# Kernel optimization log

Hardware: AMD Instinct MI355X
Metric: run time of the kernel (lower is better)

Reference implementation:

```python
import jax, jax.numpy as jnp
import numpy as np

BIT = 128
Y_P = 0.5
RIGHT = BIT / 8.0
LEFT = RIGHT / 2.0
UB = BIT / 2.0
ALPHA = 0.1
PCT_NUM, PCT_DEN = 9, 10  # percent = 9/10
C_COEF = (1.0 / RIGHT) * np.log(Y_P / (99.0 * (1.0 - Y_P)))  # slope c (constant since y_p fixed)
A_COEF = -1.0 / (LEFT * C_COEF) * np.log(99.0 * Y_P / (1.0 - Y_P))  # hard-branch factor a
# with y_p=0.5: d = -c*BP, g = -a*c*BP, so f_easy = c*(x-BP), f_hard = a*c*(x-BP)


def setup_inputs() -> dict:
    key = jax.random.key(0)
    k1, k2 = jax.random.split(key)
    N, C = 6144, 200
    u = jax.random.normal(k1, (N, BIT), dtype=jnp.float32)
    labels = jax.random.randint(k2, (N,), 0, C)
    y = jax.nn.one_hot(labels, C, dtype=jnp.int32)
    ind = jnp.arange(N, dtype=jnp.int32)  # unused dataset indices
    return {"u": u, "y": y, "ind": ind}


def reference(u, y, ind):
    sg = jax.lax.stop_gradient
    N = u.shape[0]
    uh = jnp.tanh(u)
    s = (y @ y.T) > 0                      # [N,N] bool similarity (diagonal is True)
    inner = uh @ uh.T                      # [N,N]
    n_sim = s.sum(axis=1)                  # int per-row similar count
    n_dis = N - n_sim
    fn_sim = n_sim.astype(jnp.float32)
    fn_dis = n_dis.astype(jnp.float32)
    idx = jnp.arange(N)[None, :]

    meanS = jnp.clip(jnp.where(s, inner, 0.0).sum(1) / jnp.maximum(fn_sim, 1.0), 0.0, UB)
    meanDS = jnp.clip(jnp.where(s, 0.0, inner).sum(1) / jnp.maximum(fn_dis, 1.0), 0.0, UB)

    dis_sorted = jnp.sort(jnp.where(s, -jnp.inf, inner), axis=1)
    start_dis = (n_dis * PCT_NUM) // PCT_DEN          # int(len*0.9)
    tail_mask = idx >= (N - n_dis + start_dis)[:, None]
    tail_cnt = jnp.maximum((n_dis - start_dis).astype(jnp.float32), 1.0)
    dMax = jnp.clip(jnp.where(tail_mask, dis_sorted, 0.0).sum(1) / tail_cnt, 0.0, UB)

    sim_sorted = jnp.sort(jnp.where(s, inner, jnp.inf), axis=1)
    start_sim = (n_sim * PCT_NUM) // PCT_DEN
    head_mask = idx < (n_sim - start_sim)[:, None]
    head_cnt = jnp.maximum((n_sim - start_sim).astype(jnp.float32), 1.0)
    sMin = jnp.clip(jnp.where(head_mask, sim_sorted, 0.0).sum(1) / head_cnt, 0.0, UB)

    # .item() in the original detaches these -> stop_gradient
    meanS, meanDS, dMax, sMin = map(sg, (meanS, meanDS, dMax, sMin))
    BP = meanS - (UB - meanS) / UB * jnp.abs(meanS - dMax)      # [N]
    BPd = meanDS + meanDS / UB * jnp.abs(meanDS - sMin)         # [N]

    # similar-pair loss: f + log(1+exp(-f)) == softplus(f)
    dc = inner - BP[:, None]
    f_sim = jnp.where(inner > BP[:, None], C_COEF * dc, A_COEF * C_COEF * dc)
    mask_sim = s & (inner != BP[:, None])             # == BP excluded in torch indexing
    cnt_sim = jnp.maximum(mask_sim.sum(1).astype(jnp.float32), 1.0)
    row_pos = jnp.where(mask_sim, jax.nn.softplus(f_sim), 0.0).sum(1) / cnt_sim

    # dissimilar-pair loss: log(1+exp(-f)) == softplus(-f)
    dcd = inner - BPd[:, None]
    f_dis = jnp.where(inner < BPd[:, None], C_COEF * dcd, A_COEF * C_COEF * dcd)
    mask_dis = (~s) & (inner != BPd[:, None])
    cnt_dis = jnp.maximum(mask_dis.sum(1).astype(jnp.float32), 1.0)
    row_neg = jnp.where(mask_dis, jax.nn.softplus(-f_dis), 0.0).sum(1) / cnt_dis

    valid = (n_sim > 0) & (n_dis > 0)
    count = valid.sum().astype(jnp.float32)
    posL = jnp.where(count > 0, jnp.where(valid, row_pos, 0.0).sum() / jnp.maximum(count, 1.0), 0.0)
    navL = jnp.where(count > 0, jnp.where(valid, row_neg, 0.0).sum() / jnp.maximum(count, 1.0), 0.0)

    q_loss = ALPHA * jnp.mean((uh - jnp.sign(uh)) ** 2)
    return posL + navL + q_loss
```

## Files before the change

kernel.cpp:

```cpp
#include <hip/hip_runtime.h>
#include <cstdint>

#define NROW 6144
#define KDIM 128
#define NLAB 200
#define C_COEF (-0.28719499063341177f)
#define UBV 64.0f

typedef _Float16 f16x8 __attribute__((ext_vector_type(8)));
typedef float f32x4 __attribute__((ext_vector_type(4)));
typedef __attribute__((address_space(1))) const void as1c_void;
typedef __attribute__((address_space(3))) void as3_void;

union U8 { f16x8 h; unsigned u[4]; };
union CV16 { _Float16 h; unsigned short us; };

__device__ __forceinline__ float softplus_f(float x){
  return fmaxf(x, 0.f) + __logf(1.f + __expf(-fabsf(x)));
}
__device__ __forceinline__ float waveRedF(float v){
#pragma unroll
  for (int o = 32; o; o >>= 1) v += __shfl_down(v, o, 64);
  return v;
}
__device__ __forceinline__ float bfRedF(float v){
#pragma unroll
  for (int o = 32; o; o >>= 1) v += __shfl_xor(v, o, 64);
  return v;
}
__device__ __forceinline__ int bfMaxI(int v){
#pragma unroll
  for (int o = 32; o; o >>= 1){ int x = __shfl_xor(v, o, 64); v = v > x ? v : x; }
  return v;
}
__device__ __forceinline__ float bfMaxF(float v){
#pragma unroll
  for (int o = 32; o; o >>= 1) v = fmaxf(v, __shfl_xor(v, o, 64));
  return v;
}
__device__ __forceinline__ float val_of_key(unsigned key){
  unsigned bits = (key & 0x8000u) ? (key ^ 0x8000u) : (key ^ 0xFFFFu);
  CV16 cv; cv.us = (unsigned short)bits;
  return (float)cv.h;
}

__global__ void k_label(const int* __restrict__ y, unsigned char* __restrict__ lab,
                        int* __restrict__ cnt, int* __restrict__ simIdx){
  const int row = blockIdx.x;
  const int t = threadIdx.x;
  if (t < NLAB){
    if (y[(size_t)row * NLAB + t] != 0){
      lab[row] = (unsigned char)t;
      int p = atomicAdd(&cnt[t], 1);
      if (p < 512) simIdx[t * 512 + p] = row;
    }
  }
}

__global__ __launch_bounds__(192) void k_clsmask(const unsigned char* __restrict__ lab,
                                                 unsigned* __restrict__ cm){
  const int c = blockIdx.x;
  const int w = threadIdx.x;
  const uint4* p = (const uint4*)(lab + w * 32);
  uint4 a = p[0], b = p[1];
  unsigned words[8] = {a.x, a.y, a.z, a.w, b.x, b.y, b.z, b.w};
  unsigned bits = 0;
#pragma unroll
  for (int j = 0; j < 8; j++)
#pragma unroll
    for (int i = 0; i < 4; i++)
      if (((words[j] >> (8 * i)) & 255u) == (unsigned)c) bits |= 1u << (4 * j + i);
  cm[c * 192 + w] = bits;
}

__global__ __launch_bounds__(256) void k_tanh(const float* __restrict__ u,
    _Float16* __restrict__ uhswz, float* __restrict__ accf){
  const int tid = threadIdx.x;
  const int gid = blockIdx.x * 256 + tid;
  const int row = gid >> 4;
  const int h = gid & 15;
  const int g = h ^ (row & 7);
  const float* sp = u + (size_t)row * KDIM + g * 8;
  float q = 0.f;
  f16x8 o;
#pragma unroll
  for (int t = 0; t < 8; t++){
    float x = sp[t];
    float e2 = __expf(2.f * x);
    float th = 1.f - 2.f * __builtin_amdgcn_rcpf(e2 + 1.f);
    float sg = (th > 0.f) ? 1.f : ((th < 0.f) ? -1.f : 0.f);
    float d = th - sg;
    q += d * d;
    o[t] = (_Float16)th;
  }
  *(f16x8*)(uhswz + (size_t)row * KDIM + h * 8) = o;
  q = waveRedF(q);
  __shared__ float qb[4];
  if ((tid & 63) == 0) qb[tid >> 6] = q;
  __syncthreads();
  if (tid == 0) atomicAdd(&accf[0], qb[0] + qb[1] + qb[2] + qb[3]);
}

__global__ __launch_bounds__(256) void k_mm(const _Float16* __restrict__ A,
    _Float16* __restrict__ out, int row0){
  __shared__ __align__(16) _Float16 SH[2 * 128 * KDIM];
  _Float16* As = SH;
  _Float16* Bs = SH + 128 * KDIM;
  const int tid = threadIdx.x;
  const int wav = tid >> 6, lane = tid & 63;
  const int bj = blockIdx.x, bi = blockIdx.y;

  const char* Ag = (const char*)(A + (size_t)(row0 + bi * 128) * KDIM);
  const char* Bg = (const char*)(A + (size_t)(bj * 128) * KDIM);
  char* Asb = (char*)As;
  char* Bsb = (char*)Bs;
#pragma unroll
  for (int t = 0; t < 8; t++){
    const int ub = wav * 8192 + t * 1024;
    __builtin_amdgcn_global_load_lds((as1c_void*)(Ag + ub + lane * 16),
                                     (as3_void*)(Asb + ub), 16, 0, 0);
    __builtin_amdgcn_global_load_lds((as1c_void*)(Bg + ub + lane * 16),
                                     (as3_void*)(Bsb + ub), 16, 0, 0);
  }
  __syncthreads();

  const int quad = lane >> 4, l16 = lane & 15;
  const int wm = (wav >> 1) * 64, wn = (wav & 1) * 64;
  f32x4 acc[4][4];
#pragma unroll
  for (int im = 0; im < 4; im++)
#pragma unroll
    for (int in = 0; in < 4; in++)
      acc[im][in] = (f32x4){0.f, 0.f, 0.f, 0.f};

#pragma unroll
  for (int kb = 0; kb < 4; kb++){
    f16x8 af[4], bf[4];
#pragma unroll
    for (int i = 0; i < 4; i++){
      const int m = wm + i * 16 + l16;
      const int gidx = kb * 4 + quad;
      af[i] = *(const f16x8*)(Asb + m * 256 + ((gidx ^ (m & 7)) << 4));
      const int n = wn + i * 16 + l16;
      bf[i] = *(const f16x8*)(Bsb + n * 256 + ((gidx ^ (n & 7)) << 4));
    }
#pragma unroll
    for (int im = 0; im < 4; im++)
#pragma unroll
      for (int in = 0; in < 4; in++)
        acc[im][in] = __builtin_amdgcn_mfma_f32_16x16x32_f16(af[im], bf[in], acc[im][in], 0, 0, 0);
  }
  __syncthreads();

  _Float16* Cs = SH;
#pragma unroll
  for (int im = 0; im < 4; im++)
#pragma unroll
    for (int in = 0; in < 4; in++)
#pragma unroll
      for (int r = 0; r < 4; r++){
        const int rl = wm + im * 16 + quad * 4 + r;
        const int cl = wn + in * 16 + l16;
        Cs[rl * 132 + cl] = (_Float16)acc[im][in][r];
      }
  __syncthreads();

  _Float16* obase = out + (size_t)(bi * 128) * NROW + (size_t)bj * 128;
  const int s = tid & 15;
#pragma unroll
  for (int i = 0; i < 8; i++){
    const int r = (tid >> 4) + i * 16;
    f16x8 vv = *(const f16x8*)(Cs + r * 132 + s * 8);
    *(f16x8*)(obase + (size_t)r * NROW + s * 8) = vv;
  }
}

__global__ __launch_bounds__(256) void k_stats(const _Float16* __restrict__ buf,
    const unsigned char* __restrict__ lab, const int* __restrict__ cnt,
    const int* __restrict__ simIdx, const unsigned* __restrict__ cm,
    float* __restrict__ rowRes, int row0){
  __shared__ int   histS[4][256];
  __shared__ float simvS[4][512];
  const int tid = threadIdx.x;
  const int lane = tid & 63;
  const int wav = tid >> 6;
  const int lrow = blockIdx.x * 4 + wav;
  const int row = row0 + lrow;
  const int myl = lab[row];
  const int n_sim = cnt[myl];
  const int n_dis = NROW - n_sim;
  if (n_dis == 0 || n_sim == 0) return;
  const int k1 = n_dis - (n_dis * 9) / 10;
  const int k2 = n_sim - (n_sim * 9) / 10;
  const int ns = (n_sim < 512) ? n_sim : 512;

  int*   hist = histS[wav];
  float* simv = simvS[wav];
  *(int4*)&hist[lane * 4] = make_int4(0, 0, 0, 0);

  const f16x8* src = (const f16x8*)(buf + (size_t)lrow * NROW);
  const _Float16* srcs = buf + (size_t)lrow * NROW;
  const unsigned char* mrow = (const unsigned char*)(cm + (size_t)myl * 192);

  float sumAll = 0.f;
#pragma unroll 1
  for (int it = 0; it < 12; ++it){
    U8 x; x.h = src[it * 64 + lane];
#pragma unroll
    for (int k = 0; k < 4; k++){
      unsigned wv = x.u[k];
      unsigned m = (wv >> 15) & 0x00010001u;
      unsigned key2 = wv ^ 0x80008000u ^ (m * 0x7FFFu);
      atomicAdd(&hist[(key2 >> 8) & 0xFFu], 1);
      atomicAdd(&hist[key2 >> 24], 1);
      sumAll += (float)x.h[2 * k] + (float)x.h[2 * k + 1];
    }
  }

  float sumS = 0.f;
  unsigned skey[8]; float sval[8];
#pragma unroll
  for (int j = 0; j < 8; j++){
    const int t = lane + 64 * j;
    skey[j] = 0xFFFFFFFFu; sval[j] = 0.f;
    if (t < ns){
      int idx = simIdx[myl * 512 + t];
      CV16 cv; cv.h = srcs[idx];
      unsigned bits = cv.us;
      unsigned key = bits ^ 0x8000u ^ ((bits >> 15) * 0x7FFFu);
      float v = (float)cv.h;
      simv[t] = v; sumS += v;
      atomicAdd(&hist[key >> 8], -1);
      skey[j] = key; sval[j] = v;
    }
  }
  sumAll = bfRedF(sumAll);
  sumS = bfRedF(sumS);
  const float sumD = sumAll - sumS;

  int cArr[4];
  { int4 c4 = *(const int4*)&hist[lane * 4];
    cArr[0] = c4.x; cArr[1] = c4.y; cArr[2] = c4.z; cArr[3] = c4.w; }
  int part = cArr[0] + cArr[1] + cArr[2] + cArr[3];
  int suf = part;
#pragma unroll
  for (int o = 1; o < 64; o <<= 1){
    int x = __shfl_down(suf, o, 64);
    if (lane + o < 64) suf += x;
  }
  int cum = suf - part;
  int encB = -1, krF = 0;
#pragma unroll
  for (int d = 3; d >= 0; --d){
    int cd = cArr[d];
    if (k1 > cum && k1 <= cum + cd){ encB = 4 * lane + d; krF = k1 - cum; }
    cum += cd;
  }
  const int hbStar = bfMaxI(encB);
  const int kr1 = bfMaxI(krF);

  *(int4*)&hist[lane * 4] = make_int4(0, 0, 0, 0);

  float sAb = 0.f;
#pragma unroll 1
  for (int it = 0; it < 12; ++it){
    U8 x; x.h = src[it * 64 + lane];
#pragma unroll
    for (int k = 0; k < 4; k++){
      unsigned wv = x.u[k];
      unsigned m = (wv >> 15) & 0x00010001u;
      unsigned key2 = wv ^ 0x80008000u ^ (m * 0x7FFFu);
      int hbLo = (key2 >> 8) & 0xFF;
      int hbHi = key2 >> 24;
      if (hbLo > hbStar) sAb += (float)x.h[2 * k];
      else if (hbLo == hbStar) atomicAdd(&hist[key2 & 0xFFu], 1);
      if (hbHi > hbStar) sAb += (float)x.h[2 * k + 1];
      else if (hbHi == hbStar) atomicAdd(&hist[(key2 >> 16) & 0xFFu], 1);
    }
  }
#pragma unroll
  for (int j = 0; j < 8; j++){
    if (skey[j] != 0xFFFFFFFFu){
      int hb = (int)(skey[j] >> 8);
      if (hb > hbStar) sAb -= sval[j];
      else if (hb == hbStar) atomicAdd(&hist[skey[j] & 0xFFu], -1);
    }
  }
  sAb = bfRedF(sAb);

  int c2[4];
  { int4 c4 = *(const int4*)&hist[lane * 4];
    c2[0] = c4.x; c2[1] = c4.y; c2[2] = c4.z; c2[3] = c4.w; }
  part = c2[0] + c2[1] + c2[2] + c2[3];
  suf = part;
#pragma unroll
  for (int o = 1; o < 64; o <<= 1){
    int x = __shfl_down(suf, o, 64);
    if (lane + o < 64) suf += x;
  }
  cum = suf - part;
  int encL = -1, g2F = 0;
#pragma unroll
  for (int d = 3; d >= 0; --d){
    int cd = c2[d];
    if (kr1 > cum && kr1 <= cum + cd){ encL = 4 * lane + d; g2F = cum; }
    cum += cd;
  }
  const int lbStar = bfMaxI(encL);
  const int gt2 = bfMaxI(g2F);
  float sumIn = 0.f;
#pragma unroll
  for (int d = 0; d < 4; d++){
    int lb = 4 * lane + d;
    if (lb > lbStar) sumIn += (float)c2[d] * val_of_key((unsigned)((hbStar << 8) | lb));
  }
  sumIn = bfRedF(sumIn);
  const float piv = val_of_key((unsigned)((hbStar << 8) | lbStar));
  const float dSum = sAb + sumIn + (float)(kr1 - gt2) * piv;

  float fpiv2 = -3e38f; int flt = 0;
  for (int t = lane; t < ns; t += 64){
    float vt = simv[t];
    int lt = 0, eq = 0;
    for (int j = 0; j < ns; j++){
      float vj = simv[j];
      lt += (vj < vt); eq += (vj == vt);
    }
    if (lt < k2 && k2 <= lt + eq){ fpiv2 = vt; flt = lt; }
  }
  const float piv2 = bfMaxF(fpiv2);
  const int ltS = bfMaxI(flt);
  float slt = 0.f;
  for (int t = lane; t < ns; t += 64){
    float v = simv[t];
    if (v < piv2) slt += v;
  }
  slt = bfRedF(slt);
  const float sSum = slt + (float)(k2 - ltS) * piv2;

  const float meanS  = fminf(fmaxf(sumS / fmaxf((float)n_sim, 1.f), 0.f), UBV);
  const float meanDS = fminf(fmaxf(sumD / fmaxf((float)n_dis, 1.f), 0.f), UBV);
  const float dMax   = fminf(fmaxf(dSum / fmaxf((float)k1, 1.f), 0.f), UBV);
  const float sMin   = fminf(fmaxf(sSum / fmaxf((float)k2, 1.f), 0.f), UBV);
  const float BP  = meanS - (UBV - meanS) / UBV * fabsf(meanS - dMax);
  const float BPd = meanDS + meanDS / UBV * fabsf(meanDS - sMin);

  float an = 0.f, cn = 0.f;
#pragma unroll 1
  for (int it = 0; it < 12; ++it){
    f16x8 h8 = src[it * 64 + lane];
    unsigned m8 = (unsigned)mrow[it * 64 + lane];
#pragma unroll
    for (int e = 0; e < 8; e++){
      float v = (float)h8[e];
      float dcd = v - BPd;
      float f = (v < BPd) ? C_COEF * dcd : (2.f * C_COEF) * dcd;
      float sp = softplus_f(-f);
      bool use = !((m8 >> e) & 1u) && (v != BPd);
      an += use ? sp : 0.f;
      cn += use ? 1.f : 0.f;
    }
  }
  float ap = 0.f, cp = 0.f;
  for (int t = lane; t < ns; t += 64){
    float v = simv[t];
    if (v != BP){
      float dc = v - BP;
      float f = (v > BP) ? C_COEF * dc : (2.f * C_COEF) * dc;
      ap += softplus_f(f); cp += 1.f;
    }
  }
  ap = bfRedF(ap); an = bfRedF(an);
  cp = bfRedF(cp); cn = bfRedF(cn);
  if (lane == 0){
    float4 r;
    r.x = ap / fmaxf(cp, 1.f);
    r.y = an / fmaxf(cn, 1.f);
    r.z = 1.f;
    r.w = 0.f;
    *(float4*)(rowRes + 4 * (size_t)row) = r;
  }
}

__global__ __launch_bounds__(256) void k_final(const float* __restrict__ accf,
    const float* __restrict__ rowRes, float* __restrict__ out){
  const int tid = threadIdx.x;
  float p = 0.f, n = 0.f, c = 0.f;
  for (int i = tid; i < NROW; i += 256){
    float4 r = *(const float4*)(rowRes + 4 * (size_t)i);
    p += r.x; n += r.y; c += r.z;
  }
  p = bfRedF(p); n = bfRedF(n); c = bfRedF(c);
  __shared__ float sb[12];
  const int wav = tid >> 6;
  if ((tid & 63) == 0){ sb[wav] = p; sb[4 + wav] = n; sb[8 + wav] = c; }
  __syncthreads();
  if (tid == 0){
    p = sb[0] + sb[1] + sb[2] + sb[3];
    n = sb[4] + sb[5] + sb[6] + sb[7];
    c = sb[8] + sb[9] + sb[10] + sb[11];
    float posL = 0.f, navL = 0.f;
    if (c > 0.f){ posL = p / c; navL = n / c; }
    out[0] = posL + navL + 0.1f * (accf[0] / (float)(NROW * KDIM));
  }
}

extern "C" void kernel_launch(void* const* d_in, const int* in_sizes, int n_in,
                              void* d_out, int out_size, void* d_ws, size_t ws_size,
                              hipStream_t stream){
  const float* u = (const float*)d_in[0];
  const int* y = (const int*)d_in[1];
  char* ws = (char*)d_ws;
  float* accf = (float*)ws;
  int* cnt = (int*)(ws + 64);
  unsigned char* lab = (unsigned char*)(ws + 4096);
  int* simIdx = (int*)(ws + 12288);
  unsigned* cmask = (unsigned*)(ws + 421888);
  float* rowRes = (float*)(ws + 575488);
  _Float16* uhswz = (_Float16*)(ws + 673792);
  const size_t ibufOff = 673792 + (size_t)NROW * KDIM * 2;
  _Float16* ibuf = (_Float16*)(ws + ibufOff);

  hipMemsetAsync(d_ws, 0, 673792, stream);
  k_label<<<NROW, 256, 0, stream>>>(y, lab, cnt, simIdx);
  k_clsmask<<<NLAB, 192, 0, stream>>>(lab, cmask);
  k_tanh<<<(NROW * 16) / 256, 256, 0, stream>>>(u, uhswz, accf);

  size_t avail = (ws_size > ibufOff) ? ws_size - ibufOff : 0;
  long maxRows = (long)(avail / ((size_t)NROW * 2));
  maxRows = (maxRows / 128) * 128;
  if (maxRows > NROW) maxRows = NROW;
  if (maxRows < 128) maxRows = 128;

  for (int r0 = 0; r0 < NROW; r0 += (int)maxRows){
    int rows = NROW - r0;
    if (rows > maxRows) rows = (int)maxRows;
    k_mm<<<dim3(48, rows / 128), 256, 0, stream>>>(uhswz, ibuf, r0);
    k_stats<<<rows / 4, 256, 0, stream>>>(ibuf, lab, cnt, simIdx, cmask, rowRes, r0);
  }
  k_final<<<1, 256, 0, stream>>>(accf, rowRes, (float*)d_out);
}
```

Measured before the change: 178.8 us.

## Fuse label/tanh kernels, drop class mask, split histograms, compute negatives by subtraction

Merges the label-scatter and tanh kernels into one launch and removes the class-mask kernel entirely. The dissimilar-pair loss is now summed over all entries, and the similar entries and ties are subtracted afterwards, which removes the per-element mask load. Each wave's LDS histogram is split into four padded sub-histograms to cut atomic contention. Row sums use fdot2, and the memset region shrinks. The subtraction approach adds a small floating-point cancellation risk and relies on similar entries being capped at 512 per row.

```diff
diff --git a/kernel.cpp b/kernel.cpp
--- a/kernel.cpp
+++ b/kernel.cpp
@@ -8,11 +8,12 @@
 #define UBV 64.0f
 
 typedef _Float16 f16x8 __attribute__((ext_vector_type(8)));
+typedef _Float16 f16x2 __attribute__((ext_vector_type(2)));
 typedef float f32x4 __attribute__((ext_vector_type(4)));
 typedef __attribute__((address_space(1))) const void as1c_void;
 typedef __attribute__((address_space(3))) void as3_void;
 
-union U8 { f16x8 h; unsigned u[4]; };
+union U8 { f16x8 h; unsigned u[4]; f16x2 p[4]; };
 union CV16 { _Float16 h; unsigned short us; };
 
 __device__ __forceinline__ float softplus_f(float x){
@@ -24,6 +25,11 @@
   return v;
 }
 __device__ __forceinline__ float bfRedF(float v){
+#pragma unroll
+  for (int o = 32; o; o >>= 1) v += __shfl_xor(v, o, 64);
+  return v;
+}
+__device__ __forceinline__ int bfRedI(int v){
 #pragma unroll
   for (int o = 32; o; o >>= 1) v += __shfl_xor(v, o, 64);
   return v;
@@ -44,39 +50,20 @@
   return (float)cv.h;
 }
 
-__global__ void k_label(const int* __restrict__ y, unsigned char* __restrict__ lab,
-                        int* __restrict__ cnt, int* __restrict__ simIdx){
-  const int row = blockIdx.x;
-  const int t = threadIdx.x;
-  if (t < NLAB){
-    if (y[(size_t)row * NLAB + t] != 0){
-      lab[row] = (unsigned char)t;
-      int p = atomicAdd(&cnt[t], 1);
-      if (p < 512) simIdx[t * 512 + p] = row;
-    }
-  }
-}
-
-__global__ __launch_bounds__(192) void k_clsmask(const unsigned char* __restrict__ lab,
-                                                 unsigned* __restrict__ cm){
-  const int c = blockIdx.x;
-  const int w = threadIdx.x;
-  const uint4* p = (const uint4*)(lab + w * 32);
-  uint4 a = p[0], b = p[1];
-  unsigned words[8] = {a.x, a.y, a.z, a.w, b.x, b.y, b.z, b.w};
-  unsigned bits = 0;
-#pragma unroll
-  for (int j = 0; j < 8; j++)
-#pragma unroll
-    for (int i = 0; i < 4; i++)
-      if (((words[j] >> (8 * i)) & 255u) == (unsigned)c) bits |= 1u << (4 * j + i);
-  cm[c * 192 + w] = bits;
-}
-
-__global__ __launch_bounds__(256) void k_tanh(const float* __restrict__ u,
-    _Float16* __restrict__ uhswz, float* __restrict__ accf){
+__global__ __launch_bounds__(256) void k_labtanh(const int* __restrict__ y,
+    unsigned char* __restrict__ lab, int* __restrict__ cnt, int* __restrict__ simIdx,
+    const float* __restrict__ u, _Float16* __restrict__ uhswz, float* __restrict__ accf){
+  const int bid = blockIdx.x;
   const int tid = threadIdx.x;
-  const int gid = blockIdx.x * 256 + tid;
+  if (bid < NROW){
+    if (tid < NLAB && y[(size_t)bid * NLAB + tid] != 0){
+      lab[bid] = (unsigned char)tid;
+      int p = atomicAdd(&cnt[tid], 1);
+      if (p < 512) simIdx[tid * 512 + p] = bid;
+    }
+    return;
+  }
+  const int gid = (bid - NROW) * 256 + tid;
   const int row = gid >> 4;
   const int h = gid & 15;
   const int g = h ^ (row & 7);
@@ -177,9 +164,8 @@
 
 __global__ __launch_bounds__(256) void k_stats(const _Float16* __restrict__ buf,
     const unsigned char* __restrict__ lab, const int* __restrict__ cnt,
-    const int* __restrict__ simIdx, const unsigned* __restrict__ cm,
-    float* __restrict__ rowRes, int row0){
-  __shared__ int   histS[4][256];
+    const int* __restrict__ simIdx, float* __restrict__ rowRes, int row0){
+  __shared__ int   histS[4][1028];
   __shared__ float simvS[4][512];
   const int tid = threadIdx.x;
   const int lane = tid & 63;
@@ -195,14 +181,17 @@
   const int ns = (n_sim < 512) ? n_sim : 512;
 
   int*   hist = histS[wav];
+  int*   myh  = hist + (lane >> 4) * 257;
   float* simv = simvS[wav];
-  *(int4*)&hist[lane * 4] = make_int4(0, 0, 0, 0);
+#pragma unroll
+  for (int r = 0; r < 4; r++) *(int4*)&hist[(lane + 64 * r) * 4] = make_int4(0, 0, 0, 0);
+  if (lane == 0) *(int4*)&hist[1024] = make_int4(0, 0, 0, 0);
 
   const f16x8* src = (const f16x8*)(buf + (size_t)lrow * NROW);
   const _Float16* srcs = buf + (size_t)lrow * NROW;
-  const unsigned char* mrow = (const unsigned char*)(cm + (size_t)myl * 192);
 
   float sumAll = 0.f;
+  const f16x2 ones = (f16x2){(_Float16)1.f, (_Float16)1.f};
 #pragma unroll 1
   for (int it = 0; it < 12; ++it){
     U8 x; x.h = src[it * 64 + lane];
@@ -211,36 +200,36 @@
       unsigned wv = x.u[k];
       unsigned m = (wv >> 15) & 0x00010001u;
       unsigned key2 = wv ^ 0x80008000u ^ (m * 0x7FFFu);
-      atomicAdd(&hist[(key2 >> 8) & 0xFFu], 1);
-      atomicAdd(&hist[key2 >> 24], 1);
+      atomicAdd(&myh[(key2 >> 8) & 0xFFu], 1);
+      atomicAdd(&myh[key2 >> 24], 1);
+#if __has_builtin(__builtin_amdgcn_fdot2)
+      sumAll = __builtin_amdgcn_fdot2(x.p[k], ones, sumAll, false);
+#else
       sumAll += (float)x.h[2 * k] + (float)x.h[2 * k + 1];
+#endif
     }
   }
 
   float sumS = 0.f;
-  unsigned skey[8]; float sval[8];
-#pragma unroll
-  for (int j = 0; j < 8; j++){
-    const int t = lane + 64 * j;
-    skey[j] = 0xFFFFFFFFu; sval[j] = 0.f;
-    if (t < ns){
-      int idx = simIdx[myl * 512 + t];
-      CV16 cv; cv.h = srcs[idx];
-      unsigned bits = cv.us;
-      unsigned key = bits ^ 0x8000u ^ ((bits >> 15) * 0x7FFFu);
-      float v = (float)cv.h;
-      simv[t] = v; sumS += v;
-      atomicAdd(&hist[key >> 8], -1);
-      skey[j] = key; sval[j] = v;
-    }
+  for (int t = lane; t < ns; t += 64){
+    int idx = simIdx[myl * 512 + t];
+    CV16 cv; cv.h = srcs[idx];
+    unsigned bits = (unsigned)cv.us;
+    unsigned key = bits ^ 0x8000u ^ ((bits >> 15) * 0x7FFFu);
+    float v = (float)cv.h;
+    simv[t] = v; sumS += v;
+    atomicAdd(&myh[key >> 8], -1);
   }
   sumAll = bfRedF(sumAll);
   sumS = bfRedF(sumS);
   const float sumD = sumAll - sumS;
 
   int cArr[4];
-  { int4 c4 = *(const int4*)&hist[lane * 4];
-    cArr[0] = c4.x; cArr[1] = c4.y; cArr[2] = c4.z; cArr[3] = c4.w; }
+#pragma unroll
+  for (int d = 0; d < 4; d++){
+    const int b = 4 * lane + d;
+    cArr[d] = hist[b] + hist[257 + b] + hist[514 + b] + hist[771 + b];
+  }
   int part = cArr[0] + cArr[1] + cArr[2] + cArr[3];
   int suf = part;
 #pragma unroll
@@ -259,7 +248,9 @@
   const int hbStar = bfMaxI(encB);
   const int kr1 = bfMaxI(krF);
 
-  *(int4*)&hist[lane * 4] = make_int4(0, 0, 0, 0);
+#pragma unroll
+  for (int r = 0; r < 4; r++) *(int4*)&hist[(lane + 64 * r) * 4] = make_int4(0, 0, 0, 0);
+  if (lane == 0) *(int4*)&hist[1024] = make_int4(0, 0, 0, 0);
 
   float sAb = 0.f;
 #pragma unroll 1
@@ -273,24 +264,28 @@
       int hbLo = (key2 >> 8) & 0xFF;
       int hbHi = key2 >> 24;
       if (hbLo > hbStar) sAb += (float)x.h[2 * k];
-      else if (hbLo == hbStar) atomicAdd(&hist[key2 & 0xFFu], 1);
+      else if (hbLo == hbStar) atomicAdd(&myh[key2 & 0xFFu], 1);
       if (hbHi > hbStar) sAb += (float)x.h[2 * k + 1];
-      else if (hbHi == hbStar) atomicAdd(&hist[(key2 >> 16) & 0xFFu], 1);
-    }
-  }
-#pragma unroll
-  for (int j = 0; j < 8; j++){
-    if (skey[j] != 0xFFFFFFFFu){
-      int hb = (int)(skey[j] >> 8);
-      if (hb > hbStar) sAb -= sval[j];
-      else if (hb == hbStar) atomicAdd(&hist[skey[j] & 0xFFu], -1);
-    }
+      else if (hbHi == hbStar) atomicAdd(&myh[(key2 >> 16) & 0xFFu], 1);
+    }
+  }
+  for (int t = lane; t < ns; t += 64){
+    float v = simv[t];
+    CV16 cv; cv.h = (_Float16)v;
+    unsigned bits = (unsigned)cv.us;
+    unsigned key = bits ^ 0x8000u ^ ((bits >> 15) * 0x7FFFu);
+    int hb = (int)(key >> 8);
+    if (hb > hbStar) sAb -= v;
+    else if (hb == hbStar) atomicAdd(&myh[key & 0xFFu], -1);
   }
   sAb = bfRedF(sAb);
 
   int c2[4];
-  { int4 c4 = *(const int4*)&hist[lane * 4];
-    c2[0] = c4.x; c2[1] = c4.y; c2[2] = c4.z; c2[3] = c4.w; }
+#pragma unroll
+  for (int d = 0; d < 4; d++){
+    const int b = 4 * lane + d;
+    c2[d] = hist[b] + hist[257 + b] + hist[514 + b] + hist[771 + b];
+  }
   part = c2[0] + c2[1] + c2[2] + c2[3];
   suf = part;
 #pragma unroll
@@ -345,37 +340,46 @@
   const float BP  = meanS - (UBV - meanS) / UBV * fabsf(meanS - dMax);
   const float BPd = meanDS + meanDS / UBV * fabsf(meanDS - sMin);
 
-  float an = 0.f, cn = 0.f;
+  float an = 0.f; int ties = 0;
 #pragma unroll 1
   for (int it = 0; it < 12; ++it){
     f16x8 h8 = src[it * 64 + lane];
-    unsigned m8 = (unsigned)mrow[it * 64 + lane];
 #pragma unroll
     for (int e = 0; e < 8; e++){
       float v = (float)h8[e];
       float dcd = v - BPd;
-      float f = (v < BPd) ? C_COEF * dcd : (2.f * C_COEF) * dcd;
-      float sp = softplus_f(-f);
-      bool use = !((m8 >> e) & 1u) && (v != BPd);
-      an += use ? sp : 0.f;
-      cn += use ? 1.f : 0.f;
-    }
-  }
+      float f = ((dcd < 0.f) ? C_COEF : 2.f * C_COEF) * dcd;
+      an += softplus_f(-f);
+      ties += (dcd == 0.f);
+    }
+  }
+  float spSim = 0.f; int tiesSim = 0;
   float ap = 0.f, cp = 0.f;
   for (int t = lane; t < ns; t += 64){
     float v = simv[t];
+    float dcd = v - BPd;
+    if (dcd == 0.f) tiesSim++;
+    else {
+      float f = ((dcd < 0.f) ? C_COEF : 2.f * C_COEF) * dcd;
+      spSim += softplus_f(-f);
+    }
     if (v != BP){
       float dc = v - BP;
       float f = (v > BP) ? C_COEF * dc : (2.f * C_COEF) * dc;
       ap += softplus_f(f); cp += 1.f;
     }
   }
-  ap = bfRedF(ap); an = bfRedF(an);
-  cp = bfRedF(cp); cn = bfRedF(cn);
+  an = bfRedF(an); spSim = bfRedF(spSim);
+  const int tiesT = bfRedI(ties);
+  const int tiesSimT = bfRedI(tiesSim);
+  ap = bfRedF(ap); cp = bfRedF(cp);
   if (lane == 0){
+    const float L = __logf(1.f + __expf(-0.f));
+    float anF = an - (float)tiesT * L - spSim;
+    float cnF = (float)(n_dis - (tiesT - tiesSimT));
     float4 r;
     r.x = ap / fmaxf(cp, 1.f);
-    r.y = an / fmaxf(cn, 1.f);
+    r.y = anF / fmaxf(cnF, 1.f);
     r.z = 1.f;
     r.w = 0.f;
     *(float4*)(rowRes + 4 * (size_t)row) = r;
@@ -413,18 +417,16 @@
   char* ws = (char*)d_ws;
   float* accf = (float*)ws;
   int* cnt = (int*)(ws + 64);
-  unsigned char* lab = (unsigned char*)(ws + 4096);
-  int* simIdx = (int*)(ws + 12288);
-  unsigned* cmask = (unsigned*)(ws + 421888);
-  float* rowRes = (float*)(ws + 575488);
-  _Float16* uhswz = (_Float16*)(ws + 673792);
-  const size_t ibufOff = 673792 + (size_t)NROW * KDIM * 2;
+  float* rowRes = (float*)(ws + 4096);
+  unsigned char* lab = (unsigned char*)(ws + 102400);
+  int* simIdx = (int*)(ws + 108544);
+  _Float16* uhswz = (_Float16*)(ws + 518144);
+  const size_t ibufOff = 518144 + (size_t)NROW * KDIM * 2;
   _Float16* ibuf = (_Float16*)(ws + ibufOff);
 
-  hipMemsetAsync(d_ws, 0, 673792, stream);
-  k_label<<<NROW, 256, 0, stream>>>(y, lab, cnt, simIdx);
-  k_clsmask<<<NLAB, 192, 0, stream>>>(lab, cmask);
-  k_tanh<<<(NROW * 16) / 256, 256, 0, stream>>>(u, uhswz, accf);
+  hipMemsetAsync(d_ws, 0, 102400, stream);
+  k_labtanh<<<NROW + (NROW * 16) / 256, 256, 0, stream>>>(y, lab, cnt, simIdx,
+                                                          u, uhswz, accf);
 
   size_t avail = (ws_size > ibufOff) ? ws_size - ibufOff : 0;
   long maxRows = (long)(avail / ((size_t)NROW * 2));
@@ -436,7 +438,7 @@
     int rows = NROW - r0;
     if (rows > maxRows) rows = (int)maxRows;
     k_mm<<<dim3(48, rows / 128), 256, 0, stream>>>(uhswz, ibuf, r0);
-    k_stats<<<rows / 4, 256, 0, stream>>>(ibuf, lab, cnt, simIdx, cmask, rowRes, r0);
+    k_stats<<<rows / 4, 256, 0, stream>>>(ibuf, lab, cnt, simIdx, rowRes, r0);
   }
   k_final<<<1, 256, 0, stream>>>(accf, rowRes, (float*)d_out);
 }
```

After: 170.8 us. -4.5%, faster.
